# Kernel optimization log

Hardware: AMD Instinct MI355X
Metric: run time of the kernel (lower is better)

Reference implementation:

```python
import jax, jax.numpy as jnp
import numpy as np
import math

HEADS = 8


def setup_inputs() -> dict:
    key = jax.random.key(0)
    ks = jax.random.split(key, 6)
    B, N, H, R = 16, 1024, 512, 32
    s = lambda fan_in: 1.0 / math.sqrt(fan_in)
    return {
        "x": jax.random.normal(ks[0], (B, N, H), dtype=jnp.float32),
        "Wqkv": jax.random.normal(ks[1], (H, 3 * H), dtype=jnp.float32) * s(H),
        "bqkv": jnp.zeros((3 * H,), dtype=jnp.float32),
        "Wout": jax.random.normal(ks[2], (H, H), dtype=jnp.float32) * s(H),
        "bout": jnp.zeros((H,), dtype=jnp.float32),
        "u": jax.random.normal(ks[3], (N, R), dtype=jnp.float32) * s(R),
        "v": jax.random.normal(ks[4], (R, N), dtype=jnp.float32) * s(R),
    }


def reference(x, Wqkv, bqkv, Wout, bout, u, v):
    B, N, H = x.shape
    hd = H // HEADS
    # qkv projection -> [B, N, 3, heads, head_dim] -> split
    qkv = (x @ Wqkv + bqkv).reshape(B, N, 3, HEADS, hd)
    qkv = jnp.transpose(qkv, (2, 0, 3, 1, 4))  # [3, B, heads, N, hd]
    q, k, val = qkv[0], qkv[1], qkv[2]
    # feature map applied before the softmax branch too (as in source)
    q = jax.nn.elu(q) + 1.0
    k = jax.nn.elu(k) + 1.0
    # low-rank shared bias [N, N], broadcast over batch & heads
    bias = u @ v
    scores = jnp.einsum('bhnd,bhmd->bhnm', q, k) / math.sqrt(hd)
    attn = jax.nn.softmax(scores + bias[None, None, :, :], axis=-1)
    out = jnp.einsum('bhnm,bhme->bhne', attn, val)  # [B, heads, N, hd]
    out = jnp.transpose(out, (0, 2, 1, 3)).reshape(B, N, H)
    return out @ Wout + bout
```

## Files before the change

### kernel.cpp

```cpp
#include <hip/hip_runtime.h>
#include <hip/hip_bf16.h>

typedef unsigned short u16;
typedef __attribute__((ext_vector_type(8))) short short8;
typedef __attribute__((ext_vector_type(4))) float f32x4;
typedef __attribute__((ext_vector_type(16))) float f32x16;
typedef __attribute__((ext_vector_type(4))) int i32x4;
typedef __attribute__((ext_vector_type(2))) int i32x2;

#define MFMA16(a,b,c) __builtin_amdgcn_mfma_f32_16x16x32_bf16((a),(b),(c),0,0,0)
#define MFMA32(a,b,c) __builtin_amdgcn_mfma_f32_32x32x16_bf16((a),(b),(c),0,0,0)

__device__ __forceinline__ u16 f2bf(float f) {
  union { float f; unsigned int u; } x; x.f = f;
  unsigned int u = x.u;
  return (u16)((u + 0x7fffu + ((u >> 16) & 1u)) >> 16);
}

__device__ __forceinline__ unsigned cvtpk(float a, float b) {
  unsigned r;
  asm("v_cvt_pk_bf16_f32 %0, %1, %2" : "=v"(r) : "v"(a), "v"(b));
  return r;
}

__device__ __forceinline__ float exp2v(float x) {
  float r;
  asm("v_exp_f32 %0, %1" : "=v"(r) : "v"(x));
  return r;
}

__device__ __forceinline__ void gld16(const void* g, void* l) {
  __builtin_amdgcn_global_load_lds(
      (const __attribute__((address_space(1))) void*)g,
      (__attribute__((address_space(3))) void*)l, 16, 0, 0);
}

__global__ __launch_bounds__(256) void prep(
    const float* __restrict__ x, u16* __restrict__ xb,
    const float* __restrict__ u, u16* __restrict__ ub,
    const float* __restrict__ Wqkv, u16* __restrict__ Wqkvt,
    const float* __restrict__ Wout, u16* __restrict__ Woutt,
    const float* __restrict__ vlr, u16* __restrict__ vTb) {
  __shared__ float tile[32][33];
  int bid = blockIdx.x, tid = threadIdx.x;
  if (bid < 4112) {
    const float* in; u16* out; size_t i; float sc;
    if (bid < 4096) { in = x; out = xb; i = (size_t)bid * 256 + tid; sc = 1.f; }
    else { in = u; out = ub; i = (size_t)(bid - 4096) * 256 + tid; sc = 1.44269504f; }
    f32x4 a = *(const f32x4*)(in + i * 8);
    f32x4 b = *(const f32x4*)(in + i * 8 + 4);
    union { short8 s; u16 us[8]; } r;
    #pragma unroll
    for (int j = 0; j < 4; ++j) { r.us[j] = f2bf(a[j] * sc); r.us[4 + j] = f2bf(b[j] * sc); }
    *(short8*)&out[i * 8] = r.s;
    return;
  }
  int tb = bid - 4112;
  const float* in; u16* out; int rows, cols, bx, by;
  if (tb < 768)       { in = Wqkv; out = Wqkvt; rows = 512; cols = 1536; bx = tb % 48; by = tb / 48; }
  else if (tb < 1024) { int q = tb - 768; in = Wout; out = Woutt; rows = 512; cols = 512; bx = q % 16; by = q / 16; }
  else                { in = vlr; out = vTb; rows = 32; cols = 1024; bx = tb - 1024; by = 0; }
  int bc = bx * 32, br = by * 32;
  int tx = tid & 31, ty = tid >> 5;
  #pragma unroll
  for (int i = ty; i < 32; i += 8)
    tile[i][tx] = in[(size_t)(br + i) * cols + bc + tx];
  __syncthreads();
  #pragma unroll
  for (int i = ty; i < 32; i += 8)
    out[(size_t)(bc + i) * rows + br + tx] = f2bf(tile[tx][i]);
}

__global__ __launch_bounds__(256) void vtrans(
    const u16* __restrict__ in, u16* __restrict__ out) {
  __shared__ u16 t[32][33];
  int bh = blockIdx.z;
  int n0 = blockIdx.y * 32, e0 = blockIdx.x * 32;
  int tx = threadIdx.x & 31, ty = threadIdx.x >> 5;
  size_t base = (size_t)bh << 16;
  #pragma unroll
  for (int i = ty; i < 32; i += 8)
    t[i][tx] = in[base + (size_t)(n0 + i) * 64 + e0 + tx];
  __syncthreads();
  #pragma unroll
  for (int i = ty; i < 32; i += 8)
    out[base + (size_t)(e0 + i) * 1024 + n0 + tx] = t[tx][i];
}

template<int MODE>
__global__ __launch_bounds__(256) void gemm128(
    const u16* __restrict__ A, const u16* __restrict__ Bt,
    const float* __restrict__ bias,
    u16* __restrict__ oq, u16* __restrict__ ok, u16* __restrict__ ov,
    float* __restrict__ fo) {
  const int K = 512;
  __shared__ __align__(16) u16 As[128 * 64];
  __shared__ __align__(16) u16 Bs[128 * 64];
  int tid = threadIdx.x;
  int w = tid >> 6, ln = tid & 63, lo = ln & 15, hi = ln >> 4;
  int wr = (w >> 1) * 64, wc = (w & 1) * 64;
  int lin = blockIdx.y * gridDim.x + blockIdx.x;
  int xcd = lin & 7, idx = lin >> 3;
  int perx = gridDim.x, rows_per = gridDim.y >> 3;
  int by = xcd * rows_per + idx / perx;
  int bx = idx % perx;
  int bm = by * 128, bn = bx * 128;

  f32x4 acc[4][4];
  #pragma unroll
  for (int m = 0; m < 4; ++m)
    #pragma unroll
    for (int n = 0; n < 4; ++n)
      acc[m][n] = (f32x4){0.f, 0.f, 0.f, 0.f};

  for (int k0 = 0; k0 < K; k0 += 64) {
    #pragma unroll
    for (int i = 0; i < 4; ++i) {
      int c = i * 256 + w * 64 + ln;
      int r = c >> 3, cc = c & 7;
      gld16(&A[(size_t)(bm + r) * K + k0 + ((cc ^ (r & 7)) << 3)], &As[c << 3]);
    }
    #pragma unroll
    for (int i = 0; i < 4; ++i) {
      int c = i * 256 + w * 64 + ln;
      int r = c >> 3, cc = c & 7;
      gld16(&Bt[(size_t)(bn + r) * K + k0 + ((cc ^ (r & 7)) << 3)], &Bs[c << 3]);
    }
    __syncthreads();
    #pragma unroll
    for (int ks = 0; ks < 2; ++ks) {
      short8 a[4], b[4];
      #pragma unroll
      for (int m = 0; m < 4; ++m) {
        int row = wr + m * 16 + lo;
        a[m] = *(const short8*)&As[row * 64 + (((ks * 4 + hi) ^ (lo & 7)) << 3)];
      }
      #pragma unroll
      for (int n = 0; n < 4; ++n) {
        int row = wc + n * 16 + lo;
        b[n] = *(const short8*)&Bs[row * 64 + (((ks * 4 + hi) ^ (lo & 7)) << 3)];
      }
      #pragma unroll
      for (int m = 0; m < 4; ++m)
        #pragma unroll
        for (int n = 0; n < 4; ++n)
          acc[m][n] = MFMA16(a[m], b[n], acc[m][n]);
    }
    __syncthreads();
  }
  #pragma unroll
  for (int m = 0; m < 4; ++m)
    #pragma unroll
    for (int n = 0; n < 4; ++n)
      #pragma unroll
      for (int r = 0; r < 4; ++r) {
        int row = bm + wr + m * 16 + hi * 4 + r;
        int col = bn + wc + n * 16 + lo;
        float v = acc[m][n][r] + bias[col];
        if (MODE == 0) {
          int type = col >> 9, hd = (col >> 6) & 7, e = col & 63;
          if (type < 2) {
            v = (v > 0.f) ? (v + 1.f) : __expf(v);
            if (type == 0) v *= 0.18033688f;
          }
          u16* dst = (type == 0) ? oq : ((type == 1) ? ok : ov);
          dst[(size_t)(((row >> 10) << 3) + hd) * 65536 + (size_t)(row & 1023) * 64 + e] = f2bf(v);
        } else {
          fo[(size_t)row * 512 + col] = v;
        }
      }
}

__global__ __launch_bounds__(256, 4) void attn32(
    const u16* __restrict__ qh, const u16* __restrict__ kh,
    const u16* __restrict__ vt, const u16* __restrict__ ub,
    const u16* __restrict__ vtb, u16* __restrict__ ob) {
  __shared__ __align__(16) u16 Ks[2][64 * 64];
  __shared__ __align__(16) u16 Vs[2][64 * 64];
  __shared__ __align__(16) u16 Tb[2][64 * 32];
  int tid = threadIdx.x;
  int w = tid >> 6, ln = tid & 63;
  int m32 = ln & 31, h = ln >> 5;
  int lin = blockIdx.y * 8 + blockIdx.x;
  int xcd = lin & 7, idx = lin >> 3;
  int bh = xcd * 16 + (idx >> 3);
  int q0 = (idx & 7) * 128 + w * 32;
  size_t bhb = (size_t)bh << 16;

  short8 qf[4], uf[2];
  #pragma unroll
  for (int ks = 0; ks < 4; ++ks)
    qf[ks] = *(const short8*)&qh[bhb + (size_t)(q0 + m32) * 64 + ks * 16 + h * 8];
  #pragma unroll
  for (int k2 = 0; k2 < 2; ++k2)
    uf[k2] = *(const short8*)&ub[(size_t)(q0 + m32) * 32 + k2 * 16 + h * 8];

  auto STAGE = [&](int buf, int kv) {
    #pragma unroll
    for (int i = 0; i < 2; ++i) {
      int c = i * 256 + w * 64 + ln;
      int r = c >> 3, cc = c & 7;
      gld16(&kh[bhb + (size_t)(kv + r) * 64 + ((cc ^ (r & 7)) << 3)], &Ks[buf][c << 3]);
    }
    #pragma unroll
    for (int i = 0; i < 2; ++i) {
      int c = i * 256 + w * 64 + ln;
      int r = c >> 3, cc = c & 7;
      gld16(&vt[bhb + (size_t)r * 1024 + kv + ((cc ^ (r & 7)) << 3)], &Vs[buf][c << 3]);
    }
    {
      int c = w * 64 + ln;
      int r = c >> 2, cc = c & 3;
      gld16(&vtb[(size_t)(kv + r) * 32 + ((cc ^ (r & 3)) << 3)], &Tb[buf][c << 3]);
    }
  };

  f32x16 o0 = {0.f,0.f,0.f,0.f,0.f,0.f,0.f,0.f,0.f,0.f,0.f,0.f,0.f,0.f,0.f,0.f};
  f32x16 o1 = o0;
  float mrun = -3e38f, lrun = 0.f;

  int cur = 0;
  STAGE(0, 0);
  __syncthreads();

  for (int t = 0; t < 16; ++t) {
    if (t < 15) STAGE(cur ^ 1, (t + 1) * 64);

    f32x16 s0 = {0.f,0.f,0.f,0.f,0.f,0.f,0.f,0.f,0.f,0.f,0.f,0.f,0.f,0.f,0.f,0.f};
    f32x16 s1 = s0;
    __builtin_amdgcn_s_setprio(1);
    #pragma unroll
    for (int k2 = 0; k2 < 2; ++k2) {
      int r0 = m32, r1 = 32 + m32;
      short8 t0 = *(const short8*)&Tb[cur][r0 * 32 + (((k2 * 2 + h) ^ (r0 & 3)) << 3)];
      short8 t1 = *(const short8*)&Tb[cur][r1 * 32 + (((k2 * 2 + h) ^ (r1 & 3)) << 3)];
      s0 = MFMA32(t0, uf[k2], s0);
      s1 = MFMA32(t1, uf[k2], s1);
    }
    #pragma unroll
    for (int ks = 0; ks < 4; ++ks) {
      int r0 = m32, r1 = 32 + m32;
      short8 k0f = *(const short8*)&Ks[cur][r0 * 64 + (((ks * 2 + h) ^ (r0 & 7)) << 3)];
      short8 k1f = *(const short8*)&Ks[cur][r1 * 64 + (((ks * 2 + h) ^ (r1 & 7)) << 3)];
      s0 = MFMA32(k0f, qf[ks], s0);
      s1 = MFMA32(k1f, qf[ks], s1);
    }
    __builtin_amdgcn_s_setprio(0);

    float pm = fmaxf(s0[0], s1[0]);
    #pragma unroll
    for (int i = 1; i < 16; ++i) pm = fmaxf(pm, fmaxf(s0[i], s1[i]));
    pm = fmaxf(pm, __shfl_xor(pm, 32));
    if (!__all(pm - mrun <= 11.5f)) {
      float nm = fmaxf(mrun, pm);
      float al = exp2v(mrun - nm);
      #pragma unroll
      for (int i = 0; i < 16; ++i) { o0[i] *= al; o1[i] *= al; }
      lrun *= al;
      mrun = nm;
    }
    float ls = 0.f;
    #pragma unroll
    for (int i = 0; i < 16; ++i) { float p = exp2v(s0[i] - mrun); s0[i] = p; ls += p; }
    #pragma unroll
    for (int i = 0; i < 16; ++i) { float p = exp2v(s1[i] - mrun); s1[i] = p; ls += p; }
    lrun += ls;

    unsigned pk0[4][2], pk1[4][2];
    #pragma unroll
    for (int r8 = 0; r8 < 4; ++r8) {
      pk0[r8][0] = cvtpk(s0[r8 * 4 + 0], s0[r8 * 4 + 1]);
      pk0[r8][1] = cvtpk(s0[r8 * 4 + 2], s0[r8 * 4 + 3]);
      pk1[r8][0] = cvtpk(s1[r8 * 4 + 0], s1[r8 * 4 + 1]);
      pk1[r8][1] = cvtpk(s1[r8 * 4 + 2], s1[r8 * 4 + 3]);
    }
    #pragma unroll
    for (int kvt = 0; kvt < 2; ++kvt) {
      #pragma unroll
      for (int msl = 0; msl < 2; ++msl) {
        unsigned a0 = kvt ? pk1[2 * msl][0] : pk0[2 * msl][0];
        unsigned b0 = kvt ? pk1[2 * msl + 1][0] : pk0[2 * msl + 1][0];
        unsigned a1 = kvt ? pk1[2 * msl][1] : pk0[2 * msl][1];
        unsigned b1 = kvt ? pk1[2 * msl + 1][1] : pk0[2 * msl + 1][1];
        asm("v_permlane32_swap_b32 %0, %1" : "+v"(a0), "+v"(b0));
        asm("v_permlane32_swap_b32 %0, %1" : "+v"(a1), "+v"(b1));
        union { i32x4 i; short8 s; } pu;
        pu.i = (i32x4){(int)a0, (int)a1, (int)b0, (int)b1};
        int ms = kvt * 2 + msl;
        int r0 = m32, r1 = 32 + m32;
        short8 v0 = *(const short8*)&Vs[cur][r0 * 64 + (((ms * 2 + h) ^ (r0 & 7)) << 3)];
        short8 v1 = *(const short8*)&Vs[cur][r1 * 64 + (((ms * 2 + h) ^ (r1 & 7)) << 3)];
        __builtin_amdgcn_s_setprio(1);
        o0 = MFMA32(v0, pu.s, o0);
        o1 = MFMA32(v1, pu.s, o1);
        __builtin_amdgcn_s_setprio(0);
      }
    }
    __syncthreads();
    cur ^= 1;
  }

  float lt = lrun + __shfl_xor(lrun, 32);
  float li = 1.f / lt;
  int b = bh >> 3, hd = bh & 7;
  size_t orow = ((size_t)(b * 1024 + q0 + m32)) * 512 + hd * 64;
  #pragma unroll
  for (int et = 0; et < 2; ++et) {
    #pragma unroll
    for (int r8 = 0; r8 < 4; ++r8) {
      float v0 = (et ? o1[r8 * 4 + 0] : o0[r8 * 4 + 0]) * li;
      float v1 = (et ? o1[r8 * 4 + 1] : o0[r8 * 4 + 1]) * li;
      float v2 = (et ? o1[r8 * 4 + 2] : o0[r8 * 4 + 2]) * li;
      float v3 = (et ? o1[r8 * 4 + 3] : o0[r8 * 4 + 3]) * li;
      i32x2 d = {(int)cvtpk(v0, v1), (int)cvtpk(v2, v3)};
      *(i32x2*)&ob[orow + et * 32 + 8 * r8 + 4 * h] = d;
    }
  }
}

extern "C" void kernel_launch(void* const* d_in, const int* in_sizes, int n_in,
                              void* d_out, int out_size, void* d_ws, size_t ws_size,
                              hipStream_t stream) {
  const float* x    = (const float*)d_in[0];
  const float* Wqkv = (const float*)d_in[1];
  const float* bqkv = (const float*)d_in[2];
  const float* Wout = (const float*)d_in[3];
  const float* bout = (const float*)d_in[4];
  const float* u    = (const float*)d_in[5];
  const float* vlr  = (const float*)d_in[6];
  float* out = (float*)d_out;

  char* ws = (char*)d_ws;
  u16* qh    = (u16*)(ws);
  u16* kh    = (u16*)(ws + 16777216);
  u16* xb    = (u16*)(ws + 33554432);
  u16* vTg   = (u16*)(ws + 33554432);
  u16* vtmp  = (u16*)(ws + 50331648);
  u16* ob    = (u16*)(ws + 50331648);
  u16* Wqkvt = (u16*)(ws + 67108864);
  u16* Woutt = (u16*)(ws + 68681728);
  u16* ub    = (u16*)(ws + 69206016);
  u16* vTb   = (u16*)(ws + 69271552);

  prep<<<5168, 256, 0, stream>>>(x, xb, u, ub, Wqkv, Wqkvt, Wout, Woutt, vlr, vTb);
  gemm128<0><<<dim3(12, 128), 256, 0, stream>>>(xb, Wqkvt, bqkv, qh, kh, vtmp, nullptr);
  vtrans<<<dim3(2, 32, 128), 256, 0, stream>>>(vtmp, vTg);
  attn32<<<dim3(8, 128), 256, 0, stream>>>(qh, kh, vTg, ub, vTb, ob);
  gemm128<1><<<dim3(4, 128), 256, 0, stream>>>(ob, Woutt, bout, nullptr, nullptr, nullptr, out);
}
```

Before: 220.5 us.

## Fuse V transpose into QKV GEMM epilogue and double query rows per attention wave

The QKV GEMM epilogue now writes V straight into the transposed [bh, e, n] layout with packed bf16 stores, which removes the separate vtrans kernel and its round trip through global memory. The attention kernel now gives each wave 64 query rows instead of 32, so every K/V tile loaded into LDS is reused twice as often, and the grid shrinks to half as many blocks. The low-rank bias factor tile is read directly from global memory rather than staged through LDS. The cost is roughly double the accumulator registers per wave (launch bounds drop from 4 to 2 blocks), which lowers occupancy, and the transposed V stores are strided.

```diff
diff --git a/kernel.cpp b/kernel.cpp
--- a/kernel.cpp
+++ b/kernel.cpp
@@ -69,22 +69,6 @@
   #pragma unroll
   for (int i = ty; i < 32; i += 8)
     out[(size_t)(bc + i) * rows + br + tx] = f2bf(tile[tx][i]);
-}
-
-__global__ __launch_bounds__(256) void vtrans(
-    const u16* __restrict__ in, u16* __restrict__ out) {
-  __shared__ u16 t[32][33];
-  int bh = blockIdx.z;
-  int n0 = blockIdx.y * 32, e0 = blockIdx.x * 32;
-  int tx = threadIdx.x & 31, ty = threadIdx.x >> 5;
-  size_t base = (size_t)bh << 16;
-  #pragma unroll
-  for (int i = ty; i < 32; i += 8)
-    t[i][tx] = in[base + (size_t)(n0 + i) * 64 + e0 + tx];
-  __syncthreads();
-  #pragma unroll
-  for (int i = ty; i < 32; i += 8)
-    out[base + (size_t)(e0 + i) * 1024 + n0 + tx] = t[tx][i];
 }
 
 template<int MODE>
@@ -151,49 +135,63 @@
   #pragma unroll
   for (int m = 0; m < 4; ++m)
     #pragma unroll
-    for (int n = 0; n < 4; ++n)
-      #pragma unroll
-      for (int r = 0; r < 4; ++r) {
-        int row = bm + wr + m * 16 + hi * 4 + r;
-        int col = bn + wc + n * 16 + lo;
-        float v = acc[m][n][r] + bias[col];
-        if (MODE == 0) {
-          int type = col >> 9, hd = (col >> 6) & 7, e = col & 63;
-          if (type < 2) {
+    for (int n = 0; n < 4; ++n) {
+      int col = bn + wc + n * 16 + lo;
+      int row0 = bm + wr + m * 16 + hi * 4;
+      if (MODE == 0) {
+        int type = col >> 9, hd = (col >> 6) & 7, e = col & 63;
+        float bv = bias[col];
+        if (type < 2) {
+          u16* dst = (type == 0) ? oq : ok;
+          #pragma unroll
+          for (int r = 0; r < 4; ++r) {
+            float v = acc[m][n][r] + bv;
             v = (v > 0.f) ? (v + 1.f) : __expf(v);
             if (type == 0) v *= 0.18033688f;
+            int row = row0 + r;
+            dst[(size_t)(((row >> 10) << 3) + hd) * 65536 + (size_t)(row & 1023) * 64 + e] = f2bf(v);
           }
-          u16* dst = (type == 0) ? oq : ((type == 1) ? ok : ov);
-          dst[(size_t)(((row >> 10) << 3) + hd) * 65536 + (size_t)(row & 1023) * 64 + e] = f2bf(v);
         } else {
-          fo[(size_t)row * 512 + col] = v;
+          float v0 = acc[m][n][0] + bv, v1 = acc[m][n][1] + bv;
+          float v2 = acc[m][n][2] + bv, v3 = acc[m][n][3] + bv;
+          i32x2 d = {(int)cvtpk(v0, v1), (int)cvtpk(v2, v3)};
+          int bidx = row0 >> 10;
+          *(i32x2*)&ov[(size_t)((bidx << 3) + hd) * 65536 + (size_t)e * 1024 + (row0 & 1023)] = d;
         }
-      }
-}
-
-__global__ __launch_bounds__(256, 4) void attn32(
+      } else {
+        #pragma unroll
+        for (int r = 0; r < 4; ++r)
+          fo[(size_t)(row0 + r) * 512 + col] = acc[m][n][r] + bias[col];
+      }
+    }
+}
+
+__global__ __launch_bounds__(256, 2) void attn64q(
     const u16* __restrict__ qh, const u16* __restrict__ kh,
     const u16* __restrict__ vt, const u16* __restrict__ ub,
     const u16* __restrict__ vtb, u16* __restrict__ ob) {
   __shared__ __align__(16) u16 Ks[2][64 * 64];
   __shared__ __align__(16) u16 Vs[2][64 * 64];
-  __shared__ __align__(16) u16 Tb[2][64 * 32];
   int tid = threadIdx.x;
   int w = tid >> 6, ln = tid & 63;
   int m32 = ln & 31, h = ln >> 5;
-  int lin = blockIdx.y * 8 + blockIdx.x;
+  int lin = blockIdx.y * gridDim.x + blockIdx.x;
   int xcd = lin & 7, idx = lin >> 3;
-  int bh = xcd * 16 + (idx >> 3);
-  int q0 = (idx & 7) * 128 + w * 32;
+  int bh = xcd * 16 + (idx >> 2);
+  int q0 = (idx & 3) * 256 + w * 64;
   size_t bhb = (size_t)bh << 16;
 
-  short8 qf[4], uf[2];
-  #pragma unroll
-  for (int ks = 0; ks < 4; ++ks)
-    qf[ks] = *(const short8*)&qh[bhb + (size_t)(q0 + m32) * 64 + ks * 16 + h * 8];
-  #pragma unroll
-  for (int k2 = 0; k2 < 2; ++k2)
-    uf[k2] = *(const short8*)&ub[(size_t)(q0 + m32) * 32 + k2 * 16 + h * 8];
+  short8 qf[2][4], uf[2][2];
+  #pragma unroll
+  for (int s = 0; s < 2; ++s) {
+    int qc = q0 + s * 32 + m32;
+    #pragma unroll
+    for (int ks = 0; ks < 4; ++ks)
+      qf[s][ks] = *(const short8*)&qh[bhb + (size_t)qc * 64 + ks * 16 + h * 8];
+    #pragma unroll
+    for (int k2 = 0; k2 < 2; ++k2)
+      uf[s][k2] = *(const short8*)&ub[(size_t)qc * 32 + k2 * 16 + h * 8];
+  }
 
   auto STAGE = [&](int buf, int kv) {
     #pragma unroll
@@ -201,98 +199,110 @@
       int c = i * 256 + w * 64 + ln;
       int r = c >> 3, cc = c & 7;
       gld16(&kh[bhb + (size_t)(kv + r) * 64 + ((cc ^ (r & 7)) << 3)], &Ks[buf][c << 3]);
-    }
-    #pragma unroll
-    for (int i = 0; i < 2; ++i) {
-      int c = i * 256 + w * 64 + ln;
-      int r = c >> 3, cc = c & 7;
       gld16(&vt[bhb + (size_t)r * 1024 + kv + ((cc ^ (r & 7)) << 3)], &Vs[buf][c << 3]);
     }
-    {
-      int c = w * 64 + ln;
-      int r = c >> 2, cc = c & 3;
-      gld16(&vtb[(size_t)(kv + r) * 32 + ((cc ^ (r & 3)) << 3)], &Tb[buf][c << 3]);
-    }
   };
 
-  f32x16 o0 = {0.f,0.f,0.f,0.f,0.f,0.f,0.f,0.f,0.f,0.f,0.f,0.f,0.f,0.f,0.f,0.f};
-  f32x16 o1 = o0;
-  float mrun = -3e38f, lrun = 0.f;
+  f32x16 o[2][2];
+  #pragma unroll
+  for (int s = 0; s < 2; ++s)
+    #pragma unroll
+    for (int e = 0; e < 2; ++e)
+      #pragma unroll
+      for (int i = 0; i < 16; ++i) o[s][e][i] = 0.f;
+  float mrun[2] = {-3e38f, -3e38f}, lrun[2] = {0.f, 0.f};
 
   int cur = 0;
   STAGE(0, 0);
   __syncthreads();
 
   for (int t = 0; t < 16; ++t) {
-    if (t < 15) STAGE(cur ^ 1, (t + 1) * 64);
-
-    f32x16 s0 = {0.f,0.f,0.f,0.f,0.f,0.f,0.f,0.f,0.f,0.f,0.f,0.f,0.f,0.f,0.f,0.f};
-    f32x16 s1 = s0;
+    int kv = t * 64;
+    if (t < 15) STAGE(cur ^ 1, kv + 64);
+
+    short8 tf[2][2];
+    #pragma unroll
+    for (int k2 = 0; k2 < 2; ++k2) {
+      tf[k2][0] = *(const short8*)&vtb[(size_t)(kv + m32) * 32 + k2 * 16 + h * 8];
+      tf[k2][1] = *(const short8*)&vtb[(size_t)(kv + 32 + m32) * 32 + k2 * 16 + h * 8];
+    }
+
+    f32x16 sA[2][2];
+    #pragma unroll
+    for (int s = 0; s < 2; ++s)
+      #pragma unroll
+      for (int e = 0; e < 2; ++e)
+        #pragma unroll
+        for (int i = 0; i < 16; ++i) sA[s][e][i] = 0.f;
+
     __builtin_amdgcn_s_setprio(1);
     #pragma unroll
-    for (int k2 = 0; k2 < 2; ++k2) {
-      int r0 = m32, r1 = 32 + m32;
-      short8 t0 = *(const short8*)&Tb[cur][r0 * 32 + (((k2 * 2 + h) ^ (r0 & 3)) << 3)];
-      short8 t1 = *(const short8*)&Tb[cur][r1 * 32 + (((k2 * 2 + h) ^ (r1 & 3)) << 3)];
-      s0 = MFMA32(t0, uf[k2], s0);
-      s1 = MFMA32(t1, uf[k2], s1);
-    }
+    for (int k2 = 0; k2 < 2; ++k2)
+      #pragma unroll
+      for (int s = 0; s < 2; ++s) {
+        sA[s][0] = MFMA32(tf[k2][0], uf[s][k2], sA[s][0]);
+        sA[s][1] = MFMA32(tf[k2][1], uf[s][k2], sA[s][1]);
+      }
     #pragma unroll
     for (int ks = 0; ks < 4; ++ks) {
-      int r0 = m32, r1 = 32 + m32;
-      short8 k0f = *(const short8*)&Ks[cur][r0 * 64 + (((ks * 2 + h) ^ (r0 & 7)) << 3)];
-      short8 k1f = *(const short8*)&Ks[cur][r1 * 64 + (((ks * 2 + h) ^ (r1 & 7)) << 3)];
-      s0 = MFMA32(k0f, qf[ks], s0);
-      s1 = MFMA32(k1f, qf[ks], s1);
+      short8 k0f = *(const short8*)&Ks[cur][m32 * 64 + (((ks * 2 + h) ^ (m32 & 7)) << 3)];
+      short8 k1f = *(const short8*)&Ks[cur][(32 + m32) * 64 + (((ks * 2 + h) ^ (m32 & 7)) << 3)];
+      #pragma unroll
+      for (int s = 0; s < 2; ++s) {
+        sA[s][0] = MFMA32(k0f, qf[s][ks], sA[s][0]);
+        sA[s][1] = MFMA32(k1f, qf[s][ks], sA[s][1]);
+      }
     }
     __builtin_amdgcn_s_setprio(0);
 
-    float pm = fmaxf(s0[0], s1[0]);
-    #pragma unroll
-    for (int i = 1; i < 16; ++i) pm = fmaxf(pm, fmaxf(s0[i], s1[i]));
-    pm = fmaxf(pm, __shfl_xor(pm, 32));
-    if (!__all(pm - mrun <= 11.5f)) {
-      float nm = fmaxf(mrun, pm);
-      float al = exp2v(mrun - nm);
-      #pragma unroll
-      for (int i = 0; i < 16; ++i) { o0[i] *= al; o1[i] *= al; }
-      lrun *= al;
-      mrun = nm;
-    }
-    float ls = 0.f;
-    #pragma unroll
-    for (int i = 0; i < 16; ++i) { float p = exp2v(s0[i] - mrun); s0[i] = p; ls += p; }
-    #pragma unroll
-    for (int i = 0; i < 16; ++i) { float p = exp2v(s1[i] - mrun); s1[i] = p; ls += p; }
-    lrun += ls;
-
-    unsigned pk0[4][2], pk1[4][2];
-    #pragma unroll
-    for (int r8 = 0; r8 < 4; ++r8) {
-      pk0[r8][0] = cvtpk(s0[r8 * 4 + 0], s0[r8 * 4 + 1]);
-      pk0[r8][1] = cvtpk(s0[r8 * 4 + 2], s0[r8 * 4 + 3]);
-      pk1[r8][0] = cvtpk(s1[r8 * 4 + 0], s1[r8 * 4 + 1]);
-      pk1[r8][1] = cvtpk(s1[r8 * 4 + 2], s1[r8 * 4 + 3]);
-    }
-    #pragma unroll
-    for (int kvt = 0; kvt < 2; ++kvt) {
-      #pragma unroll
-      for (int msl = 0; msl < 2; ++msl) {
-        unsigned a0 = kvt ? pk1[2 * msl][0] : pk0[2 * msl][0];
-        unsigned b0 = kvt ? pk1[2 * msl + 1][0] : pk0[2 * msl + 1][0];
-        unsigned a1 = kvt ? pk1[2 * msl][1] : pk0[2 * msl][1];
-        unsigned b1 = kvt ? pk1[2 * msl + 1][1] : pk0[2 * msl + 1][1];
+    unsigned pk[2][2][4][2];
+    #pragma unroll
+    for (int s = 0; s < 2; ++s) {
+      float pm = fmaxf(sA[s][0][0], sA[s][0][1]);
+      #pragma unroll
+      for (int i = 2; i < 16; i += 2) pm = fmaxf(fmaxf(pm, sA[s][0][i]), sA[s][0][i + 1]);
+      #pragma unroll
+      for (int i = 0; i < 16; i += 2) pm = fmaxf(fmaxf(pm, sA[s][1][i]), sA[s][1][i + 1]);
+      pm = fmaxf(pm, __shfl_xor(pm, 32));
+      if (!__all(pm - mrun[s] <= 11.5f)) {
+        float nm = fmaxf(mrun[s], pm);
+        float al = exp2v(mrun[s] - nm);
+        #pragma unroll
+        for (int i = 0; i < 16; ++i) { o[s][0][i] *= al; o[s][1][i] *= al; }
+        lrun[s] *= al;
+        mrun[s] = nm;
+      }
+      float ls = 0.f;
+      #pragma unroll
+      for (int i = 0; i < 16; ++i) { float p = exp2v(sA[s][0][i] - mrun[s]); sA[s][0][i] = p; ls += p; }
+      #pragma unroll
+      for (int i = 0; i < 16; ++i) { float p = exp2v(sA[s][1][i] - mrun[s]); sA[s][1][i] = p; ls += p; }
+      lrun[s] += ls;
+      #pragma unroll
+      for (int hf = 0; hf < 2; ++hf)
+        #pragma unroll
+        for (int r8 = 0; r8 < 4; ++r8) {
+          pk[s][hf][r8][0] = cvtpk(sA[s][hf][r8 * 4 + 0], sA[s][hf][r8 * 4 + 1]);
+          pk[s][hf][r8][1] = cvtpk(sA[s][hf][r8 * 4 + 2], sA[s][hf][r8 * 4 + 3]);
+        }
+    }
+
+    #pragma unroll
+    for (int ms = 0; ms < 4; ++ms) {
+      int kvt = ms >> 1, msl = ms & 1;
+      short8 v0 = *(const short8*)&Vs[cur][m32 * 64 + (((ms * 2 + h) ^ (m32 & 7)) << 3)];
+      short8 v1 = *(const short8*)&Vs[cur][(32 + m32) * 64 + (((ms * 2 + h) ^ (m32 & 7)) << 3)];
+      #pragma unroll
+      for (int s = 0; s < 2; ++s) {
+        unsigned a0 = pk[s][kvt][2 * msl][0], b0 = pk[s][kvt][2 * msl + 1][0];
+        unsigned a1 = pk[s][kvt][2 * msl][1], b1 = pk[s][kvt][2 * msl + 1][1];
         asm("v_permlane32_swap_b32 %0, %1" : "+v"(a0), "+v"(b0));
         asm("v_permlane32_swap_b32 %0, %1" : "+v"(a1), "+v"(b1));
-        union { i32x4 i; short8 s; } pu;
+        union { i32x4 i; short8 s8; } pu;
         pu.i = (i32x4){(int)a0, (int)a1, (int)b0, (int)b1};
-        int ms = kvt * 2 + msl;
-        int r0 = m32, r1 = 32 + m32;
-        short8 v0 = *(const short8*)&Vs[cur][r0 * 64 + (((ms * 2 + h) ^ (r0 & 7)) << 3)];
-        short8 v1 = *(const short8*)&Vs[cur][r1 * 64 + (((ms * 2 + h) ^ (r1 & 7)) << 3)];
         __builtin_amdgcn_s_setprio(1);
-        o0 = MFMA32(v0, pu.s, o0);
-        o1 = MFMA32(v1, pu.s, o1);
+        o[s][0] = MFMA32(v0, pu.s8, o[s][0]);
+        o[s][1] = MFMA32(v1, pu.s8, o[s][1]);
         __builtin_amdgcn_s_setprio(0);
       }
     }
@@ -300,21 +310,23 @@
     cur ^= 1;
   }
 
-  float lt = lrun + __shfl_xor(lrun, 32);
-  float li = 1.f / lt;
   int b = bh >> 3, hd = bh & 7;
-  size_t orow = ((size_t)(b * 1024 + q0 + m32)) * 512 + hd * 64;
-  #pragma unroll
-  for (int et = 0; et < 2; ++et) {
-    #pragma unroll
-    for (int r8 = 0; r8 < 4; ++r8) {
-      float v0 = (et ? o1[r8 * 4 + 0] : o0[r8 * 4 + 0]) * li;
-      float v1 = (et ? o1[r8 * 4 + 1] : o0[r8 * 4 + 1]) * li;
-      float v2 = (et ? o1[r8 * 4 + 2] : o0[r8 * 4 + 2]) * li;
-      float v3 = (et ? o1[r8 * 4 + 3] : o0[r8 * 4 + 3]) * li;
-      i32x2 d = {(int)cvtpk(v0, v1), (int)cvtpk(v2, v3)};
-      *(i32x2*)&ob[orow + et * 32 + 8 * r8 + 4 * h] = d;
-    }
+  #pragma unroll
+  for (int s = 0; s < 2; ++s) {
+    float lt = lrun[s] + __shfl_xor(lrun[s], 32);
+    float li = 1.f / lt;
+    size_t orow = ((size_t)(b * 1024 + q0 + s * 32 + m32)) * 512 + hd * 64;
+    #pragma unroll
+    for (int et = 0; et < 2; ++et)
+      #pragma unroll
+      for (int r8 = 0; r8 < 4; ++r8) {
+        float v0 = o[s][et][r8 * 4 + 0] * li;
+        float v1 = o[s][et][r8 * 4 + 1] * li;
+        float v2 = o[s][et][r8 * 4 + 2] * li;
+        float v3 = o[s][et][r8 * 4 + 3] * li;
+        i32x2 d = {(int)cvtpk(v0, v1), (int)cvtpk(v2, v3)};
+        *(i32x2*)&ob[orow + et * 32 + 8 * r8 + 4 * h] = d;
+      }
   }
 }
 
@@ -334,17 +346,15 @@
   u16* qh    = (u16*)(ws);
   u16* kh    = (u16*)(ws + 16777216);
   u16* xb    = (u16*)(ws + 33554432);
-  u16* vTg   = (u16*)(ws + 33554432);
-  u16* vtmp  = (u16*)(ws + 50331648);
-  u16* ob    = (u16*)(ws + 50331648);
+  u16* ob    = (u16*)(ws + 33554432);
+  u16* vTg   = (u16*)(ws + 50331648);
   u16* Wqkvt = (u16*)(ws + 67108864);
   u16* Woutt = (u16*)(ws + 68681728);
   u16* ub    = (u16*)(ws + 69206016);
   u16* vTb   = (u16*)(ws + 69271552);
 
   prep<<<5168, 256, 0, stream>>>(x, xb, u, ub, Wqkv, Wqkvt, Wout, Woutt, vlr, vTb);
-  gemm128<0><<<dim3(12, 128), 256, 0, stream>>>(xb, Wqkvt, bqkv, qh, kh, vtmp, nullptr);
-  vtrans<<<dim3(2, 32, 128), 256, 0, stream>>>(vtmp, vTg);
-  attn32<<<dim3(8, 128), 256, 0, stream>>>(qh, kh, vTg, ub, vTb, ob);
+  gemm128<0><<<dim3(12, 128), 256, 0, stream>>>(xb, Wqkvt, bqkv, qh, kh, vTg, nullptr);
+  attn64q<<<dim3(4, 128), 256, 0, stream>>>(qh, kh, vTg, ub, vTb, ob);
   gemm128<1><<<dim3(4, 128), 256, 0, stream>>>(ob, Woutt, bout, nullptr, nullptr, nullptr, out);
 }
```

Result: faster. 207.4 us (-6.0%).
